# Kernel tuning notes

Hardware: AMD Instinct MI355X
Metric: run time of the kernel (lower is better)

## Reference

```python
import jax, jax.numpy as jnp
import numpy as np

N_NODES = 100000
N_EDGES = 1600000
IN_DIM = 512
HID = 64
OUT_DIM = 5


def _gcn_conv(x, row, col, w, W, b, n_nodes):
    """PyG GCNConv: h = x @ W; out[col] += norm * h[row]; out += b.
    norm = deg^-1/2[row] * w * deg^-1/2[col], deg from edge weights scattered on col,
    with self-loops (weight 1) already appended by caller."""
    h = x @ W  # [N, F_out]
    deg = jax.ops.segment_sum(w, col, num_segments=n_nodes)  # [N]
    dinv = jnp.where(deg > 0, jax.lax.rsqrt(deg), 0.0)
    norm = dinv[row] * w * dinv[col]  # [E']
    msg = h[row] * norm[:, None]  # [E', F_out] edge-wise gather + scale
    out = jax.ops.segment_sum(msg, col, num_segments=n_nodes)  # scatter-add
    return out + b


def setup_inputs() -> dict:
    key = jax.random.key(0)
    ks = jax.random.split(key, 10)
    x = jax.random.normal(ks[0], (N_NODES, IN_DIM), dtype=jnp.float32)
    edge_index = jax.random.randint(ks[1], (2, N_EDGES), 0, N_NODES, dtype=jnp.int32)
    edge_attr = jax.random.uniform(ks[2], (N_EDGES,), dtype=jnp.float32)
    # Glorot-ish init for params
    W1 = jax.random.normal(ks[3], (IN_DIM, HID), dtype=jnp.float32) * (1.0 / np.sqrt(IN_DIM))
    b1 = jnp.zeros((HID,), dtype=jnp.float32)
    W2 = jax.random.normal(ks[4], (HID, HID), dtype=jnp.float32) * (1.0 / np.sqrt(HID))
    b2 = jnp.zeros((HID,), dtype=jnp.float32)
    Wfc = jax.random.normal(ks[5], (HID, OUT_DIM), dtype=jnp.float32) * (1.0 / np.sqrt(HID))
    bfc = jnp.zeros((OUT_DIM,), dtype=jnp.float32)
    return {"x": x, "edge_index": edge_index, "edge_attr": edge_attr,
            "W1": W1, "b1": b1, "W2": W2, "b2": b2, "Wfc": Wfc, "bfc": bfc}


def reference(x, edge_index, edge_attr, W1, b1, W2, b2, Wfc, bfc):
    n = x.shape[0]
    loop = jnp.arange(n, dtype=edge_index.dtype)
    row = jnp.concatenate([edge_index[0], loop])  # source nodes + self-loops
    col = jnp.concatenate([edge_index[1], loop])  # target nodes + self-loops
    w = jnp.concatenate([edge_attr, jnp.ones((n,), dtype=edge_attr.dtype)])
    h = jax.nn.relu(_gcn_conv(x, row, col, w, W1, b1, n))
    # dropout(p=0.5) is identity in eval/reference mode
    h = jax.nn.relu(_gcn_conv(h, row, col, w, W2, b2, n))
    return h @ Wfc + bfc
```

## Files before the change

### kernel.cpp

```cpp
#include <hip/hip_runtime.h>

#define HID 64
#define OUTD 5
#define BCAP 16384
#define PART_CHUNK 4096

typedef __attribute__((ext_vector_type(8))) short bf16x8;
typedef __attribute__((ext_vector_type(4))) float f32x4;

__device__ inline void split_bf16(float x, short& hi, short& lo) {
    unsigned u = __float_as_uint(x);
    unsigned h = u >> 16;
    float hf = __uint_as_float(h << 16);
    float lof = x - hf;
    unsigned l = __float_as_uint(lof) >> 16;
    hi = (short)h; lo = (short)l;
}

__device__ inline ushort f2bf(float x) {
    unsigned u = __float_as_uint(x);
    u += 0x7fffu + ((u >> 16) & 1u);
    return (ushort)(u >> 16);
}
__device__ inline float bf2f(ushort b) {
    return __uint_as_float(((unsigned)b) << 16);
}

__global__ void k_prep(const float* __restrict__ W1, const float* __restrict__ W2,
                       short* __restrict__ w1hi, short* __restrict__ w1lo,
                       short* __restrict__ w2hi, short* __restrict__ w2lo,
                       int* __restrict__ gcursor, int nbuck) {
    int gid = blockIdx.x * blockDim.x + threadIdx.x;
    if (gid < nbuck) gcursor[gid] = 0;
    if (gid >= 32768 + 4096) return;
    int which = (gid >= 32768);
    int g = which ? gid - 32768 : gid;
    const float* W = which ? W2 : W1;
    short* ph = which ? w2hi : w1hi;
    short* pl = which ? w2lo : w1lo;
    int b = g & 7, lane = (g >> 3) & 63, c = (g >> 9) & 3, s = g >> 11;
    int k = s * 32 + 8 * (lane >> 4) + b;
    int j = c * 16 + (lane & 15);
    float x = W[k * 64 + j];
    short hi, lo; split_bf16(x, hi, lo);
    ph[g] = hi; pl[g] = lo;
}

template<int K>
__device__ inline void gemm_body(const float* __restrict__ A,
                                 const short* __restrict__ whi,
                                 const short* __restrict__ wlo,
                                 ushort* __restrict__ C, int M, int bid, int tid) {
    const int NS = K / 32;
    int lane = tid & 63;
    int wave = tid >> 6;
    int r0 = bid * 128 + wave * 32;

    int ar0 = r0 + (lane & 15);      if (ar0 >= M) ar0 = M - 1;
    int ar1 = r0 + 16 + (lane & 15); if (ar1 >= M) ar1 = M - 1;
    const float* pa0 = A + (size_t)ar0 * K + 8 * (lane >> 4);
    const float* pa1 = A + (size_t)ar1 * K + 8 * (lane >> 4);
    const bf16x8* bh = (const bf16x8*)whi + lane;
    const bf16x8* bl = (const bf16x8*)wlo + lane;

    f32x4 acc[2][4];
    #pragma unroll
    for (int r = 0; r < 2; r++)
        #pragma unroll
        for (int c = 0; c < 4; c++) acc[r][c] = (f32x4){0.f, 0.f, 0.f, 0.f};

    #pragma unroll
    for (int s = 0; s < NS; s++) {
        float4 x0 = *(const float4*)(pa0 + s * 32);
        float4 x1 = *(const float4*)(pa0 + s * 32 + 4);
        float4 y0 = *(const float4*)(pa1 + s * 32);
        float4 y1 = *(const float4*)(pa1 + s * 32 + 4);
        float xs[8] = {x0.x, x0.y, x0.z, x0.w, x1.x, x1.y, x1.z, x1.w};
        float ys[8] = {y0.x, y0.y, y0.z, y0.w, y1.x, y1.y, y1.z, y1.w};
        bf16x8 ah0, al0, ah1, al1;
        #pragma unroll
        for (int e = 0; e < 8; e++) {
            short h, l;
            split_bf16(xs[e], h, l); ah0[e] = h; al0[e] = l;
            split_bf16(ys[e], h, l); ah1[e] = h; al1[e] = l;
        }
        #pragma unroll
        for (int c = 0; c < 4; c++) {
            bf16x8 wh = bh[(s * 4 + c) * 64];
            bf16x8 wl = bl[(s * 4 + c) * 64];
            acc[0][c] = __builtin_amdgcn_mfma_f32_16x16x32_bf16(ah0, wh, acc[0][c], 0, 0, 0);
            acc[0][c] = __builtin_amdgcn_mfma_f32_16x16x32_bf16(ah0, wl, acc[0][c], 0, 0, 0);
            acc[0][c] = __builtin_amdgcn_mfma_f32_16x16x32_bf16(al0, wh, acc[0][c], 0, 0, 0);
            acc[1][c] = __builtin_amdgcn_mfma_f32_16x16x32_bf16(ah1, wh, acc[1][c], 0, 0, 0);
            acc[1][c] = __builtin_amdgcn_mfma_f32_16x16x32_bf16(ah1, wl, acc[1][c], 0, 0, 0);
            acc[1][c] = __builtin_amdgcn_mfma_f32_16x16x32_bf16(al1, wh, acc[1][c], 0, 0, 0);
        }
    }

    #pragma unroll
    for (int r = 0; r < 2; r++) {
        #pragma unroll
        for (int reg = 0; reg < 4; reg++) {
            int grow = r0 + r * 16 + 4 * (lane >> 4) + reg;
            if (grow < M) {
                #pragma unroll
                for (int c = 0; c < 4; c++)
                    C[(size_t)grow * 64 + c * 16 + (lane & 15)] = f2bf(acc[r][c][reg]);
            }
        }
    }
}

__global__ __launch_bounds__(256) void k_fused1(const float* __restrict__ x,
                                                const short* __restrict__ w1hi,
                                                const short* __restrict__ w1lo,
                                                ushort* __restrict__ h1, int M, int gGemm,
                                                const int* __restrict__ row,
                                                const int* __restrict__ col,
                                                const float* __restrict__ ea,
                                                int* __restrict__ gcursor,
                                                int2* __restrict__ bucket_mem,
                                                int nbuck, int E) {
    __shared__ int sh[512];
    int bid = blockIdx.x;
    int t = threadIdx.x;
    if (bid < gGemm) {
        gemm_body<512>(x, w1hi, w1lo, h1, M, bid, t);
        return;
    }
    int* hist = sh;
    int* basearr = sh + 256;
    int pb = bid - gGemm;
    int e0 = pb * PART_CHUNK;
    if (t < nbuck) hist[t] = 0;
    __syncthreads();
    int cols[PART_CHUNK / 256];
    #pragma unroll
    for (int i = 0; i < PART_CHUNK / 256; i++) {
        int e = e0 + t + i * 256;
        cols[i] = (e < E) ? col[e] : -1;
        if (cols[i] >= 0) atomicAdd(&hist[cols[i] >> 9], 1);
    }
    __syncthreads();
    if (t < nbuck) {
        basearr[t] = atomicAdd(&gcursor[t], hist[t]);
        hist[t] = 0;
    }
    __syncthreads();
    #pragma unroll
    for (int i = 0; i < PART_CHUNK / 256; i++) {
        int e = e0 + t + i * 256;
        if (e < E) {
            int c = cols[i];
            int b = c >> 9;
            int pos = basearr[b] + atomicAdd(&hist[b], 1);
            if (pos < BCAP) {
                int pack = ((c & 511) << 17) | row[e];
                bucket_mem[(size_t)b * BCAP + pos] = make_int2(pack, __float_as_int(ea[e]));
            }
        }
    }
}

__global__ __launch_bounds__(256) void k_build(const int* __restrict__ gcursor,
                                               const int2* __restrict__ bucket_mem,
                                               int2* __restrict__ edges,
                                               int2* __restrict__ nodemeta,
                                               float* __restrict__ dinv, int n) {
    __shared__ int hcnt[512];
    __shared__ int hoff[512];
    __shared__ float hdeg[512];
    __shared__ int ps[256];
    int b = blockIdx.x;
    int t = threadIdx.x;
    int cntb = gcursor[b]; if (cntb > BCAP) cntb = BCAP;
    const int2* bm = bucket_mem + (size_t)b * BCAP;

    #pragma unroll
    for (int l = t; l < 512; l += 256) { hcnt[l] = 0; hdeg[l] = 0.f; }
    __syncthreads();
    for (int i = t; i < cntb; i += 256) atomicAdd(&hcnt[bm[i].x >> 17], 1);
    __syncthreads();
    int a0 = hcnt[2 * t], a1 = hcnt[2 * t + 1];
    ps[t] = a0 + a1;
    __syncthreads();
    for (int o = 1; o < 256; o <<= 1) {
        int v = (t >= o) ? ps[t - o] : 0;
        __syncthreads();
        ps[t] += v;
        __syncthreads();
    }
    int excl = ps[t] - (a0 + a1);
    hoff[2 * t] = excl;
    hoff[2 * t + 1] = excl + a0;
    __syncthreads();
    #pragma unroll
    for (int l = t; l < 512; l += 256) hcnt[l] = 0;
    __syncthreads();
    for (int i = t; i < cntb; i += 256) {
        int2 eM = bm[i];
        int local = eM.x >> 17;
        int src = eM.x & 0x1FFFF;
        int p = hoff[local] + atomicAdd(&hcnt[local], 1);
        edges[(size_t)b * BCAP + p] = make_int2(src, eM.y);
        atomicAdd(&hdeg[local], __int_as_float(eM.y));
    }
    __syncthreads();
    #pragma unroll
    for (int l = t; l < 512; l += 256) {
        int node = b * 512 + l;
        if (node < n) {
            nodemeta[node] = make_int2(b * BCAP + hoff[l], hcnt[l]);
            dinv[node] = rsqrtf(hdeg[l] + 1.0f);
        }
    }
}

__global__ void k_norm(const int2* __restrict__ nodemeta, int2* __restrict__ edges,
                       const float* __restrict__ dinv, int n) {
    int gw = (blockIdx.x * blockDim.x + threadIdx.x) >> 6;
    int lane = threadIdx.x & 63;
    if (gw >= n) return;
    int2 meta = nodemeta[gw];
    int2* seg = edges + meta.x;
    for (int i = lane; i < meta.y; i += 64) {
        int2 c = seg[i];
        c.y = __float_as_int(dinv[c.x] * __int_as_float(c.y));
        seg[i] = c;
    }
}

template<int FC>
__global__ void k_gather(const ushort* __restrict__ h, const int2* __restrict__ nodemeta,
                         const int2* __restrict__ edges, const float* __restrict__ dinv,
                         const float* __restrict__ bias, const float* __restrict__ Wfc,
                         const float* __restrict__ bfc, float* __restrict__ out, int n) {
    int gw = (blockIdx.x * blockDim.x + threadIdx.x) >> 6;
    int lane = threadIdx.x & 63;
    if (gw >= n) return;
    int2 meta = nodemeta[gw];
    int cnt = meta.y;
    const int2* seg = edges + meta.x;
    float self = bf2f(h[(size_t)gw * 64 + lane]);
    float dvc = dinv[gw];
    float acc = 0.f;
    int i = 0;
    for (; i + 8 <= cnt; i += 8) {
        int4 p0 = *(const int4*)(seg + i);
        int4 p1 = *(const int4*)(seg + i + 2);
        int4 p2 = *(const int4*)(seg + i + 4);
        int4 p3 = *(const int4*)(seg + i + 6);
        float v0 = bf2f(h[(size_t)p0.x * 64 + lane]);
        float v1 = bf2f(h[(size_t)p0.z * 64 + lane]);
        float v2 = bf2f(h[(size_t)p1.x * 64 + lane]);
        float v3 = bf2f(h[(size_t)p1.z * 64 + lane]);
        float v4 = bf2f(h[(size_t)p2.x * 64 + lane]);
        float v5 = bf2f(h[(size_t)p2.z * 64 + lane]);
        float v6 = bf2f(h[(size_t)p3.x * 64 + lane]);
        float v7 = bf2f(h[(size_t)p3.z * 64 + lane]);
        float s0 = __int_as_float(p0.y) * v0 + __int_as_float(p0.w) * v1;
        float s1 = __int_as_float(p1.y) * v2 + __int_as_float(p1.w) * v3;
        float s2 = __int_as_float(p2.y) * v4 + __int_as_float(p2.w) * v5;
        float s3 = __int_as_float(p3.y) * v6 + __int_as_float(p3.w) * v7;
        acc += (s0 + s1) + (s2 + s3);
    }
    for (; i < cnt; i++) {
        int2 c = seg[i];
        acc += __int_as_float(c.y) * bf2f(h[(size_t)c.x * 64 + lane]);
    }
    acc = dvc * acc + dvc * dvc * self + bias[lane];
    acc = fmaxf(acc, 0.f);
    if (FC == 0) {
        out[(size_t)gw * 64 + lane] = acc;
    } else {
        float res = 0.f;
        #pragma unroll
        for (int j = 0; j < OUTD; j++) {
            float p = acc * Wfc[lane * OUTD + j];
            #pragma unroll
            for (int o = 1; o < 64; o <<= 1) p += __shfl_xor(p, o);
            if (lane == j) res = p;
        }
        if (lane < OUTD) out[(size_t)gw * OUTD + lane] = res + bfc[lane];
    }
}

__global__ __launch_bounds__(256) void k_gemm2(const float* __restrict__ A,
                                               const short* __restrict__ whi,
                                               const short* __restrict__ wlo,
                                               ushort* __restrict__ C, int M) {
    gemm_body<64>(A, whi, wlo, C, M, blockIdx.x, threadIdx.x);
}

extern "C" void kernel_launch(void* const* d_in, const int* in_sizes, int n_in,
                              void* d_out, int out_size, void* d_ws, size_t ws_size,
                              hipStream_t stream) {
    const float* x   = (const float*)d_in[0];
    const int*   ei  = (const int*)d_in[1];
    const float* ea  = (const float*)d_in[2];
    const float* W1  = (const float*)d_in[3];
    const float* b1  = (const float*)d_in[4];
    const float* W2  = (const float*)d_in[5];
    const float* b2  = (const float*)d_in[6];
    const float* Wfc = (const float*)d_in[7];
    const float* bfc = (const float*)d_in[8];

    const int N = in_sizes[0] / 512;
    const int E = in_sizes[1] / 2;
    const int nbuck = (N + 511) >> 9;

    const int* row = ei;
    const int* col = ei + E;

    uintptr_t p = (uintptr_t)d_ws;
    auto carve = [&](size_t bytes) -> void* {
        void* r = (void*)p;
        p += (bytes + 255) & ~(size_t)255;
        return r;
    };
    int*    gcursor    = (int*)carve((size_t)nbuck * 4);
    float*  dinv       = (float*)carve((size_t)N * 4);
    int2*   nodemeta   = (int2*)carve((size_t)N * 8);
    int2*   bucket_mem = (int2*)carve((size_t)nbuck * BCAP * 8);
    int2*   edges      = (int2*)carve((size_t)nbuck * BCAP * 8);
    short*  w1hi       = (short*)carve(32768 * 2);
    short*  w1lo       = (short*)carve(32768 * 2);
    short*  w2hi       = (short*)carve(4096 * 2);
    short*  w2lo       = (short*)carve(4096 * 2);
    ushort* hbuf       = (ushort*)carve((size_t)N * 64 * 2);
    float*  gbuf       = (float*)carve((size_t)N * 64 * 4);
    (void)ws_size;

    const int B = 256;
    int gGemm = (N + 127) / 128;
    int gPart = (E + PART_CHUNK - 1) / PART_CHUNK;
    int gWave = (N * 64 + B - 1) / B;
    int gPrep = (32768 + 4096 + B - 1) / B;

    k_prep<<<gPrep, B, 0, stream>>>(W1, W2, w1hi, w1lo, w2hi, w2lo, gcursor, nbuck);
    k_fused1<<<gGemm + gPart, B, 0, stream>>>(x, w1hi, w1lo, hbuf, N, gGemm,
                                              row, col, ea, gcursor, bucket_mem, nbuck, E);
    k_build<<<nbuck, B, 0, stream>>>(gcursor, bucket_mem, edges, nodemeta, dinv, N);
    k_norm<<<gWave, B, 0, stream>>>(nodemeta, edges, dinv, N);
    k_gather<0><<<gWave, B, 0, stream>>>(hbuf, nodemeta, edges, dinv, b1,
                                         nullptr, nullptr, gbuf, N);
    k_gemm2<<<gGemm, B, 0, stream>>>(gbuf, w2hi, w2lo, hbuf, N);
    k_gather<1><<<gWave, B, 0, stream>>>(hbuf, nodemeta, edges, dinv, b2,
                                         Wfc, bfc, (float*)d_out, N);
}
```

Baseline: 284.0 us.

## Pad per-node edge lists to multiples of 16 for fully unrolled gathers

```diff
diff --git a/kernel.cpp b/kernel.cpp
--- a/kernel.cpp
+++ b/kernel.cpp
@@ -181,8 +181,9 @@
     __syncthreads();
     for (int i = t; i < cntb; i += 256) atomicAdd(&hcnt[bm[i].x >> 17], 1);
     __syncthreads();
-    int a0 = hcnt[2 * t], a1 = hcnt[2 * t + 1];
-    ps[t] = a0 + a1;
+    int c0 = hcnt[2 * t], c1 = hcnt[2 * t + 1];
+    int q0 = (c0 + 15) & ~15, q1 = (c1 + 15) & ~15;
+    ps[t] = q0 + q1;
     __syncthreads();
     for (int o = 1; o < 256; o <<= 1) {
         int v = (t >= o) ? ps[t - o] : 0;
@@ -190,9 +191,9 @@
         ps[t] += v;
         __syncthreads();
     }
-    int excl = ps[t] - (a0 + a1);
+    int excl = ps[t] - (q0 + q1);
     hoff[2 * t] = excl;
-    hoff[2 * t + 1] = excl + a0;
+    hoff[2 * t + 1] = excl + q0;
     __syncthreads();
     #pragma unroll
     for (int l = t; l < 512; l += 256) hcnt[l] = 0;
@@ -210,7 +211,11 @@
     for (int l = t; l < 512; l += 256) {
         int node = b * 512 + l;
         if (node < n) {
-            nodemeta[node] = make_int2(b * BCAP + hoff[l], hcnt[l]);
+            int cnt = hcnt[l];
+            int pc = (cnt + 15) & ~15;
+            for (int p2 = cnt; p2 < pc; p2++)
+                edges[(size_t)b * BCAP + hoff[l] + p2] = make_int2(node, 0);
+            nodemeta[node] = make_int2(b * BCAP + hoff[l], pc);
             dinv[node] = rsqrtf(hdeg[l] + 1.0f);
         }
     }
@@ -244,30 +249,60 @@
     float self = bf2f(h[(size_t)gw * 64 + lane]);
     float dvc = dinv[gw];
     float acc = 0.f;
-    int i = 0;
-    for (; i + 8 <= cnt; i += 8) {
-        int4 p0 = *(const int4*)(seg + i);
-        int4 p1 = *(const int4*)(seg + i + 2);
-        int4 p2 = *(const int4*)(seg + i + 4);
-        int4 p3 = *(const int4*)(seg + i + 6);
-        float v0 = bf2f(h[(size_t)p0.x * 64 + lane]);
-        float v1 = bf2f(h[(size_t)p0.z * 64 + lane]);
-        float v2 = bf2f(h[(size_t)p1.x * 64 + lane]);
-        float v3 = bf2f(h[(size_t)p1.z * 64 + lane]);
-        float v4 = bf2f(h[(size_t)p2.x * 64 + lane]);
-        float v5 = bf2f(h[(size_t)p2.z * 64 + lane]);
-        float v6 = bf2f(h[(size_t)p3.x * 64 + lane]);
-        float v7 = bf2f(h[(size_t)p3.z * 64 + lane]);
-        float s0 = __int_as_float(p0.y) * v0 + __int_as_float(p0.w) * v1;
-        float s1 = __int_as_float(p1.y) * v2 + __int_as_float(p1.w) * v3;
-        float s2 = __int_as_float(p2.y) * v4 + __int_as_float(p2.w) * v5;
-        float s3 = __int_as_float(p3.y) * v6 + __int_as_float(p3.w) * v7;
-        acc += (s0 + s1) + (s2 + s3);
-    }
-    for (; i < cnt; i++) {
-        int2 c = seg[i];
-        acc += __int_as_float(c.y) * bf2f(h[(size_t)c.x * 64 + lane]);
-    }
+
+    if (cnt == 16) {
+        int4 p[8];
+        #pragma unroll
+        for (int q = 0; q < 8; q++) p[q] = *(const int4*)(seg + 2 * q);
+        float v[16];
+        #pragma unroll
+        for (int q = 0; q < 8; q++) {
+            v[2 * q]     = bf2f(h[(size_t)p[q].x * 64 + lane]);
+            v[2 * q + 1] = bf2f(h[(size_t)p[q].z * 64 + lane]);
+        }
+        #pragma unroll
+        for (int q = 0; q < 8; q++)
+            acc += __int_as_float(p[q].y) * v[2 * q] + __int_as_float(p[q].w) * v[2 * q + 1];
+    } else if (cnt == 32) {
+        int4 pA[8], pB[8];
+        #pragma unroll
+        for (int q = 0; q < 8; q++) pA[q] = *(const int4*)(seg + 2 * q);
+        #pragma unroll
+        for (int q = 0; q < 8; q++) pB[q] = *(const int4*)(seg + 16 + 2 * q);
+        float vA[16], vB[16];
+        #pragma unroll
+        for (int q = 0; q < 8; q++) {
+            vA[2 * q]     = bf2f(h[(size_t)pA[q].x * 64 + lane]);
+            vA[2 * q + 1] = bf2f(h[(size_t)pA[q].z * 64 + lane]);
+        }
+        #pragma unroll
+        for (int q = 0; q < 8; q++) {
+            vB[2 * q]     = bf2f(h[(size_t)pB[q].x * 64 + lane]);
+            vB[2 * q + 1] = bf2f(h[(size_t)pB[q].z * 64 + lane]);
+        }
+        #pragma unroll
+        for (int q = 0; q < 8; q++)
+            acc += __int_as_float(pA[q].y) * vA[2 * q] + __int_as_float(pA[q].w) * vA[2 * q + 1];
+        #pragma unroll
+        for (int q = 0; q < 8; q++)
+            acc += __int_as_float(pB[q].y) * vB[2 * q] + __int_as_float(pB[q].w) * vB[2 * q + 1];
+    } else {
+        for (int i = 0; i < cnt; i += 16) {
+            int4 p[8];
+            #pragma unroll
+            for (int q = 0; q < 8; q++) p[q] = *(const int4*)(seg + i + 2 * q);
+            float v[16];
+            #pragma unroll
+            for (int q = 0; q < 8; q++) {
+                v[2 * q]     = bf2f(h[(size_t)p[q].x * 64 + lane]);
+                v[2 * q + 1] = bf2f(h[(size_t)p[q].z * 64 + lane]);
+            }
+            #pragma unroll
+            for (int q = 0; q < 8; q++)
+                acc += __int_as_float(p[q].y) * v[2 * q] + __int_as_float(p[q].w) * v[2 * q + 1];
+        }
+    }
+
     acc = dvc * acc + dvc * dvc * self + bias[lane];
     acc = fmaxf(acc, 0.f);
     if (FC == 0) {
```

New measurement: 282.6 us. No clear change (-0.5%).
